# Kernel optimization log

Measured on AMD Instinct MI355X. Metric: run time of the kernel, lower is better.

Reference implementation:

```python
import jax, jax.numpy as jnp
import numpy as np

NV, NH = 6000, 6000
DV, DH = 1024, 1024
HID, HEADS = 128, 3
EV, EH, EC = 200000, 200000, 32768


def _gat(x, ei, W, a_src, a_dst, bias, edge_attr=None, lin_e=None, a_e=None):
    """PyG GATConv (heads=H, concat=False, add_self_loops=True, LeakyReLU 0.2).
    Returns (node_out [N,C], alpha [E+N, H])."""
    N = x.shape[0]
    H, C = a_src.shape
    xw = (x @ W).reshape(N, H, C)                      # [N,H,C]
    asrc = jnp.einsum('nhc,hc->nh', xw, a_src)         # [N,H]
    adst = jnp.einsum('nhc,hc->nh', xw, a_dst)
    loop = jnp.arange(N, dtype=ei.dtype)               # self-loops appended
    src = jnp.concatenate([ei[0], loop])
    dst = jnp.concatenate([ei[1], loop])
    alpha = asrc[src] + adst[dst]                      # [E+N,H]
    if edge_attr is not None:
        # edge_dim=1 path: lin_edge(weight)[E,H,C] dotted with att_edge; self-loop attr = mean (PyG fill_value='mean')
        ea = jnp.concatenate([edge_attr, jnp.full((N,), jnp.mean(edge_attr), edge_attr.dtype)])
        ef = (ea[:, None] * lin_e[None, :]).reshape(-1, H, C)
        alpha = alpha + jnp.einsum('ehc,hc->eh', ef, a_e)
    alpha = jax.nn.leaky_relu(alpha, 0.2)
    # segment softmax over incoming edges of each destination node
    amax = jax.ops.segment_max(alpha, dst, num_segments=N)
    ex = jnp.exp(alpha - amax[dst])
    den = jax.ops.segment_sum(ex, dst, num_segments=N)
    alpha = ex / (den[dst] + 1e-16)
    out = jax.ops.segment_sum(xw[src] * alpha[..., None], dst, num_segments=N)
    return out.mean(axis=1) + bias, alpha              # concat=False -> head mean


def _bn(x, g, b):  # BatchNorm1d, training mode (batch stats, biased var)
    m = x.mean(0)
    v = x.var(0)
    return (x - m) / jnp.sqrt(v + 1e-5) * g + b


def reference(virus_data, host_data, coexistence_data, virus_edge_weight, host_edge_weight,
              vW, v_asrc, v_adst, v_bias, v_line, v_atte,
              hW, h_asrc, h_adst, h_bias, h_line, h_atte,
              vhW, vh_asrc, vh_adst, vh_bias,
              hvW, hv_asrc, hv_adst, hv_bias,
              linv_W, linv_b, linh_W, linh_b, bn_g, bn_b,
              virus_edge_index, host_edge_index, coexistence_edge_index, coexistence_edge_index_t):
    feat_v, alpha_v = _gat(virus_data, virus_edge_index, vW, v_asrc, v_adst, v_bias,
                           virus_edge_weight, v_line, v_atte)
    feat_h, alpha_h = _gat(host_data, host_edge_index, hW, h_asrc, h_adst, h_bias,
                           host_edge_weight, h_line, h_atte)
    feat_vh, alpha_vh = _gat(coexistence_data, coexistence_edge_index_t, vhW, vh_asrc, vh_adst, vh_bias)
    feat_hv, alpha_hv = _gat(coexistence_data.T, coexistence_edge_index, hvW, hv_asrc, hv_adst, hv_bias)

    vh = jax.nn.leaky_relu(_bn(virus_data @ linv_W + linv_b, bn_g, bn_b), 0.01)
    hh = jax.nn.leaky_relu(_bn(host_data @ linh_W + linh_b, bn_g, bn_b), 0.01)

    output_host = vh @ hh.T                  # [Nv,Nh]
    output_virus = (hh @ vh.T).T             # [Nv,Nh]
    return (output_host, output_virus, output_host + output_virus,
            alpha_v, alpha_h, alpha_vh, alpha_hv,
            feat_v, feat_h, feat_vh, feat_hv)


def setup_inputs() -> dict:
    key = jax.random.key(0)
    ks = iter(jax.random.split(key, 48))

    def nrm(shape, s=0.05):
        return (jax.random.normal(next(ks), shape, jnp.float32) * s).astype(jnp.float32)

    def gat_params(din, edge=True):
        p = [nrm((din, HEADS * HID)), nrm((HEADS, HID)), nrm((HEADS, HID)), jnp.zeros((HID,), jnp.float32)]
        if edge:
            p += [nrm((HEADS * HID,)), nrm((HEADS, HID))]
        return p

    inp = {
        'virus_data': jax.random.normal(next(ks), (NV, DV), jnp.float32),
        'host_data': jax.random.normal(next(ks), (NH, DH), jnp.float32),
        'coexistence_data': jax.random.normal(next(ks), (DV, DH), jnp.float32),
        'virus_edge_weight': jax.random.uniform(next(ks), (EV,), jnp.float32),
        'host_edge_weight': jax.random.uniform(next(ks), (EH,), jnp.float32),
    }
    for pref, din, edge in [('v', DV, True), ('h', DH, True)]:
        W, asrc, adst, b, le, ae = gat_params(din, True)
        inp.update({f'{pref}W': W, f'{pref}_asrc': asrc, f'{pref}_adst': adst,
                    f'{pref}_bias': b, f'{pref}_line': le, f'{pref}_atte': ae})
    for pref, din in [('vh', DH), ('hv', DV)]:
        W, asrc, adst, b = gat_params(din, False)
        inp.update({f'{pref}W': W, f'{pref}_asrc': asrc, f'{pref}_adst': adst, f'{pref}_bias': b})
    inp.update({
        'linv_W': nrm((DV, HID)), 'linv_b': jnp.zeros((HID,), jnp.float32),
        'linh_W': nrm((DH, HID)), 'linh_b': jnp.zeros((HID,), jnp.float32),
        'bn_g': jnp.ones((HID,), jnp.float32), 'bn_b': jnp.zeros((HID,), jnp.float32),
        'virus_edge_index': jax.random.randint(next(ks), (2, EV), 0, NV, jnp.int32),
        'host_edge_index': jax.random.randint(next(ks), (2, EH), 0, NH, jnp.int32),
        'coexistence_edge_index': jax.random.randint(next(ks), (2, EC), 0, DH, jnp.int32),
        'coexistence_edge_index_t': jax.random.randint(next(ks), (2, EC), 0, DV, jnp.int32),
    })
    return inp
```

## Files before the change

kernel.cpp:

```cpp
#include <hip/hip_runtime.h>

#define NV   6000
#define NH   6000
#define EV   200000
#define EH   200000
#define EC   32768
#define GCAP 256

typedef __attribute__((ext_vector_type(8))) short bf16x8;
typedef __attribute__((ext_vector_type(4))) float f32x4;

__device__ __forceinline__ unsigned short f2bf(float f){
  unsigned u = __float_as_uint(f);
  u += 0x7FFFu + ((u >> 16) & 1u);
  return (unsigned short)(u >> 16);
}
__device__ __forceinline__ float bf2f(unsigned short h){
  return __uint_as_float((unsigned)h << 16);
}

__global__ __launch_bounds__(256) void k0(
    const float* __restrict__ vW, const float* __restrict__ v_as, const float* __restrict__ v_ad,
    const float* __restrict__ hW, const float* __restrict__ h_as, const float* __restrict__ h_ad,
    const float* __restrict__ vhW, const float* __restrict__ vh_as, const float* __restrict__ vh_ad,
    const float* __restrict__ hvW, const float* __restrict__ hv_as, const float* __restrict__ hv_ad,
    const float* __restrict__ vew, const float* __restrict__ hew,
    const float* __restrict__ v_line, const float* __restrict__ v_atte,
    const float* __restrict__ h_line, const float* __restrict__ h_atte,
    const int* __restrict__ vdst, const int* __restrict__ hdst,
    const int* __restrict__ c1dst, const int* __restrict__ c2dst,
    float* WasV, float* WadV, float* WasH, float* WadH,
    float* WasC1, float* WadC1, float* WasC2, float* WadC2,
    float* sums, float* Kbuf,
    int* cntV, int* cntH, int* cntC1, int* cntC2)
{
  __shared__ float red4[4][2];
  int b = blockIdx.x, t = threadIdx.x;
  int lane = t & 63, w = t >> 6;

  if (b < 2048){
    int m = b >> 9;
    int krow = (b & 511) * 2 + (t >> 7);
    int c = t & 127;
    const float *W, *as_, *ad_; float *Was, *Wad;
    switch (m){
      case 0:  W=vW;  as_=v_as;  ad_=v_ad;  Was=WasV;  Wad=WadV;  break;
      case 1:  W=hW;  as_=h_as;  ad_=h_ad;  Was=WasH;  Wad=WadH;  break;
      case 2:  W=vhW; as_=vh_as; ad_=vh_ad; Was=WasC1; Wad=WadC1; break;
      default: W=hvW; as_=hv_as; ad_=hv_ad; Was=WasC2; Wad=WadC2; break;
    }
    const float* Wr = W + (size_t)krow * 384;
    for (int h = 0; h < 3; h++){
      float x = Wr[h*128 + c];
      float s = x * as_[h*128 + c], d = x * ad_[h*128 + c];
      for (int off = 32; off > 0; off >>= 1){ s += __shfl_down(s, off); d += __shfl_down(d, off); }
      if (lane == 0){ red4[w][0] = s; red4[w][1] = d; }
      __syncthreads();
      if (t == 0)  { Was[krow*3+h] = red4[0][0] + red4[1][0]; Wad[krow*3+h] = red4[0][1] + red4[1][1]; }
      if (t == 128){ Was[krow*3+h] = red4[2][0] + red4[3][0]; Wad[krow*3+h] = red4[2][1] + red4[3][1]; }
      __syncthreads();
    }
    return;
  }
  b -= 2048;
  if (b < 1819){
    int idx = b * 256 + t;
    if (idx >= EV + EH + 2*EC) return;
    const int* dp; int* cnt; int e;
    if      (idx < EV)       { dp=vdst;  cnt=cntV;  e=idx; }
    else if (idx < EV+EH)    { dp=hdst;  cnt=cntH;  e=idx-EV; }
    else if (idx < EV+EH+EC) { dp=c1dst; cnt=cntC1; e=idx-EV-EH; }
    else                     { dp=c2dst; cnt=cntC2; e=idx-EV-EH-EC; }
    atomicAdd(&cnt[dp[e]], 1);
    return;
  }
  b -= 1819;
  if (b < 256){
    int which = b >> 7, base = b & 127;
    const float* x = which ? hew : vew;
    float s = 0.f;
    for (int i = base*256 + t; i < EV; i += 128*256) s += x[i];
    for (int off = 32; off > 0; off >>= 1) s += __shfl_down(s, off);
    if (lane == 0) red4[w][0] = s;
    __syncthreads();
    if (t == 0) atomicAdd(&sums[which], red4[0][0]+red4[1][0]+red4[2][0]+red4[3][0]);
    return;
  }
  for (int h = 0; h < 3; h++){
    float s = (t < 128) ? v_line[h*128+t] * v_atte[h*128+t] : 0.f;
    for (int off = 32; off > 0; off >>= 1) s += __shfl_down(s, off);
    if (lane == 0) red4[w][0] = s;
    __syncthreads();
    if (t == 0) Kbuf[h] = red4[0][0]+red4[1][0]+red4[2][0]+red4[3][0];
    __syncthreads();
    s = (t < 128) ? h_line[h*128+t] * h_atte[h*128+t] : 0.f;
    for (int off = 32; off > 0; off >>= 1) s += __shfl_down(s, off);
    if (lane == 0) red4[w][0] = s;
    __syncthreads();
    if (t == 0) Kbuf[3+h] = red4[0][0]+red4[1][0]+red4[2][0]+red4[3][0];
    __syncthreads();
  }
}

__global__ __launch_bounds__(256) void k_prep(
    const float* __restrict__ virus, const float* __restrict__ hostd, const float* __restrict__ coex,
    const float* __restrict__ vW, const float* __restrict__ linvW,
    const float* __restrict__ hW, const float* __restrict__ linhW,
    const float* __restrict__ vhW, const float* __restrict__ hvW,
    const float* __restrict__ WasV, const float* __restrict__ WadV,
    const float* __restrict__ WasH, const float* __restrict__ WadH,
    const float* __restrict__ WasC1, const float* __restrict__ WadC1,
    const float* __restrict__ WasC2, const float* __restrict__ WadC2,
    int* cntV, int* startsV, int* cntH, int* startsH,
    int* cntC1, int* startsC1, int* cntC2, int* startsC2,
    unsigned short* Avb, unsigned short* Ahb, unsigned short* Acb,
    unsigned short* Actb, unsigned short* BtV, unsigned short* BtH,
    unsigned short* BtVH, unsigned short* BtHV,
    float* asV, float* adV, float* asH, float* adH,
    float* asC1, float* adC1, float* asC2, float* adC2)
{
  __shared__ float scratch[64*65];
  int b = blockIdx.x, t = threadIdx.x;
  int lane = t & 63, w = t >> 6;

  if (b < 13024){
    const float* x; unsigned short* dstp; const float* Was; const float* Wad;
    float* ao; float* doo; int row;
    if (b < 6000)       { row=b;       x=virus; dstp=Avb; Was=WasV;  Wad=WadV;  ao=asV;  doo=adV; }
    else if (b < 12000) { row=b-6000;  x=hostd; dstp=Ahb; Was=WasH;  Wad=WadH;  ao=asH;  doo=adH; }
    else                { row=b-12000; x=coex;  dstp=Acb; Was=WasC1; Wad=WadC1; ao=asC1; doo=adC1; }
    float4 v = reinterpret_cast<const float4*>(x + (size_t)row * 1024)[t];
    ushort4 o; o.x = f2bf(v.x); o.y = f2bf(v.y); o.z = f2bf(v.z); o.w = f2bf(v.w);
    reinterpret_cast<ushort4*>(dstp + (size_t)row * 1024)[t] = o;
    const float4* Wp = reinterpret_cast<const float4*>(Was + t*12);
    float4 wa = Wp[0], wb = Wp[1], wcc = Wp[2];
    const float4* Dp = reinterpret_cast<const float4*>(Wad + t*12);
    float4 da = Dp[0], db = Dp[1], dcc = Dp[2];
    float r[6];
    r[0] = v.x*wa.x + v.y*wa.w + v.z*wb.z + v.w*wcc.y;
    r[1] = v.x*wa.y + v.y*wb.x + v.z*wb.w + v.w*wcc.z;
    r[2] = v.x*wa.z + v.y*wb.y + v.z*wcc.x + v.w*wcc.w;
    r[3] = v.x*da.x + v.y*da.w + v.z*db.z + v.w*dcc.y;
    r[4] = v.x*da.y + v.y*db.x + v.z*db.w + v.w*dcc.z;
    r[5] = v.x*da.z + v.y*db.y + v.z*dcc.x + v.w*dcc.w;
    for (int off = 32; off > 0; off >>= 1)
#pragma unroll
      for (int i = 0; i < 6; i++) r[i] += __shfl_down(r[i], off);
    float (*sh6)[6] = (float(*)[6])scratch;
    if (lane == 0)
#pragma unroll
      for (int i = 0; i < 6; i++) sh6[w][i] = r[i];
    __syncthreads();
    if (t < 6){
      float s = sh6[0][t] + sh6[1][t] + sh6[2][t] + sh6[3][t];
      if (t < 3) ao[row*3 + t] = s; else doo[row*3 + (t-3)] = s;
    }
    return;
  }
  b -= 13024;
  if (b < 704){
    float (*tp_lds)[65] = (float(*)[65])scratch;
    const float* src; unsigned short* dst; int Nc, roff, ntn, rel;
    if      (b < 256){ src=coex;  dst=Actb; Nc=1024; roff=0;   ntn=16; rel=b; }
    else if (b < 352){ src=vW;    dst=BtV;  Nc=384;  roff=0;   ntn=6;  rel=b-256; }
    else if (b < 384){ src=linvW; dst=BtV;  Nc=128;  roff=384; ntn=2;  rel=b-352; }
    else if (b < 480){ src=hW;    dst=BtH;  Nc=384;  roff=0;   ntn=6;  rel=b-384; }
    else if (b < 512){ src=linhW; dst=BtH;  Nc=128;  roff=384; ntn=2;  rel=b-480; }
    else if (b < 608){ src=vhW;   dst=BtVH; Nc=384;  roff=0;   ntn=6;  rel=b-512; }
    else             { src=hvW;   dst=BtHV; Nc=384;  roff=0;   ntn=6;  rel=b-608; }
    int tn = rel % ntn, tk = rel / ntn;
    int k0_ = tk * 64, n0 = tn * 64;
    int tx = t & 63, ty = t >> 6;
#pragma unroll
    for (int r = 0; r < 16; r++)
      tp_lds[ty + r*4][tx] = src[(size_t)(k0_ + ty + r*4) * Nc + n0 + tx];
    __syncthreads();
#pragma unroll
    for (int r = 0; r < 16; r++)
      dst[(size_t)(n0 + ty + r*4 + roff) * 1024 + k0_ + tx] = f2bf(tp_lds[tx][ty + r*4]);
    return;
  }
  b -= 704;
  if (b < 32){
    float (*st)[32][6] = (float(*)[32][6])scratch;
    int c = t & 31, ks = t >> 5;
    int nn = b * 32 + c;
    float a[6] = {0,0,0,0,0,0};
    for (int k = ks*128; k < ks*128 + 128; k++){
      float xv = coex[(size_t)k*1024 + nn];
      a[0] += xv*WasC2[k*3+0]; a[1] += xv*WasC2[k*3+1]; a[2] += xv*WasC2[k*3+2];
      a[3] += xv*WadC2[k*3+0]; a[4] += xv*WadC2[k*3+1]; a[5] += xv*WadC2[k*3+2];
    }
#pragma unroll
    for (int j = 0; j < 6; j++) st[ks][c][j] = a[j];
    __syncthreads();
    if (t < 32){
      float r[6] = {0,0,0,0,0,0};
#pragma unroll
      for (int k = 0; k < 8; k++)
#pragma unroll
        for (int j = 0; j < 6; j++) r[j] += st[k][t][j];
      int n2 = b * 32 + t;
      asC2[n2*3] = r[0]; asC2[n2*3+1] = r[1]; asC2[n2*3+2] = r[2];
      adC2[n2*3] = r[3]; adC2[n2*3+1] = r[4]; adC2[n2*3+2] = r[5];
    }
    return;
  }
  b -= 32;
  int* ssc = (int*)scratch;
  int* cnt; int* st_; int N;
  switch (b){
    case 0:  cnt=cntV;  st_=startsV;  N=NV;   break;
    case 1:  cnt=cntH;  st_=startsH;  N=NH;   break;
    case 2:  cnt=cntC1; st_=startsC1; N=1024; break;
    default: cnt=cntC2; st_=startsC2; N=1024; break;
  }
  int chunk = (N + 255) >> 8;
  int lo = t * chunk, hi = lo + chunk;
  if (hi > N) hi = N;
  if (lo > N) lo = N;
  int s = 0;
  for (int i = lo; i < hi; i++) s += cnt[i];
  ssc[t] = s;
  __syncthreads();
  for (int off = 1; off < 256; off <<= 1){
    int v = (t >= off) ? ssc[t - off] : 0;
    __syncthreads();
    ssc[t] += v;
    __syncthreads();
  }
  int run = ssc[t] - s;
  for (int i = lo; i < hi; i++){ st_[i] = run; run += cnt[i]; }
  if (t == 255) st_[N] = ssc[255];
}

template<int MODE>
__device__ __forceinline__ void gemm_body(
    const unsigned short* __restrict__ A, const unsigned short* __restrict__ B,
    int M, int N, unsigned short* __restrict__ xwb, float* __restrict__ lin,
    int bx, int by)
{
  const int tid  = threadIdx.x;
  const int lane = tid & 63, w = tid >> 6;
  const int wr = w >> 1, wc = w & 1;
  const int R  = by * 128 + wr * 64;
  const int Cb = bx * 64 + wc * 32;
  const int r0 = lane & 15, kg = lane >> 4;

  const unsigned short* pa[4]; const unsigned short* pb[2];
  bool va[4], vb[2];
#pragma unroll
  for (int i = 0; i < 4; i++){
    int row = R + i * 16 + r0;
    va[i] = row < M;
    pa[i] = A + (size_t)(va[i] ? row : 0) * 1024 + kg * 8;
  }
#pragma unroll
  for (int j = 0; j < 2; j++){
    int col = Cb + j * 16 + r0;
    vb[j] = col < N;
    pb[j] = B + (size_t)(vb[j] ? col : 0) * 1024 + kg * 8;
  }
  const bf16x8 Z8 = {0,0,0,0,0,0,0,0};
  f32x4 acc[4][2];
#pragma unroll
  for (int i = 0; i < 4; i++)
#pragma unroll
    for (int j = 0; j < 2; j++) acc[i][j] = (f32x4){0.f,0.f,0.f,0.f};

  for (int kk = 0; kk < 1024; kk += 32){
    bf16x8 av[4], bv[2];
#pragma unroll
    for (int i = 0; i < 4; i++){
      bf16x8 ta = *reinterpret_cast<const bf16x8*>(pa[i] + kk);
      av[i] = va[i] ? ta : Z8;
    }
#pragma unroll
    for (int j = 0; j < 2; j++){
      bf16x8 tb = *reinterpret_cast<const bf16x8*>(pb[j] + kk);
      bv[j] = vb[j] ? tb : Z8;
    }
#pragma unroll
    for (int i = 0; i < 4; i++)
#pragma unroll
      for (int j = 0; j < 2; j++)
        acc[i][j] = __builtin_amdgcn_mfma_f32_16x16x32_bf16(av[i], bv[j], acc[i][j], 0, 0, 0);
  }

  const int cn = lane & 15, rq = (lane >> 4) * 4;
#pragma unroll
  for (int i = 0; i < 4; i++){
    int row0 = R + i * 16 + rq;
#pragma unroll
    for (int j = 0; j < 2; j++){
      int col = Cb + j * 16 + cn;
      if (col < N){
#pragma unroll
        for (int r = 0; r < 4; r++){
          int row = row0 + r;
          if (row < M){
            float v = acc[i][j][r];
            if (MODE == 0){
              if (col < 384) xwb[(size_t)row * 384 + col] = f2bf(v);
              else           lin[(size_t)row * 128 + col - 384] = v;
            } else {
              xwb[(size_t)row * 384 + col] = f2bf(v);
            }
          }
        }
      }
    }
  }
}

__global__ __launch_bounds__(256) void k_sg(
    const unsigned short* Avb, const unsigned short* BtV, unsigned short* xwbV, float* linV,
    const unsigned short* Ahb, const unsigned short* BtH, unsigned short* xwbH, float* linH,
    const unsigned short* Acb,  const unsigned short* BtVH, unsigned short* xwbC1,
    const unsigned short* Actb, const unsigned short* BtHV, unsigned short* xwbC2,
    const int* vdst, const int* hdst, const int* c1dst, const int* c2dst,
    const int* stV, const int* stH, const int* st1, const int* st2,
    int* cuV, int* cuH, int* cu1, int* cu2,
    int* soV, int* soH, int* so1, int* so2)
{
  int b = blockIdx.x;
  if (b < 848){
    if (b < 376)       gemm_body<0>(Avb,  BtV,  NV,   512, xwbV,  linV, b & 7, b >> 3);
    else if (b < 752){ int g = b - 376; gemm_body<0>(Ahb,  BtH,  NH,   512, xwbH,  linH, g & 7, g >> 3); }
    else if (b < 800){ int g = b - 752; gemm_body<1>(Acb,  BtVH, 1024, 384, xwbC1, nullptr, g % 6, g / 6); }
    else             { int g = b - 800; gemm_body<1>(Actb, BtHV, 1024, 384, xwbC2, nullptr, g % 6, g / 6); }
    return;
  }
  int idx = (b - 848) * 256 + threadIdx.x;
  if (idx >= EV + EH + 2*EC) return;
  const int* dp; const int* st; int* cur; int* so; int e;
  if      (idx < EV)       { dp=vdst;  st=stV; cur=cuV; so=soV; e=idx; }
  else if (idx < EV+EH)    { dp=hdst;  st=stH; cur=cuH; so=soH; e=idx-EV; }
  else if (idx < EV+EH+EC) { dp=c1dst; st=st1; cur=cu1; so=so1; e=idx-EV-EH; }
  else                     { dp=c2dst; st=st2; cur=cu2; so=so2; e=idx-EV-EH-EC; }
  int d = dp[e];
  so[st[d] + atomicAdd(&cur[d], 1)] = e;
}

struct GatDesc {
  const unsigned short* xwb; const int* src; const int* sorted; const int* starts;
  const float* as_; const float* ad_; const float* Kc; const float* ew; const float* sumw;
  const float* bias; float* alpha; float* feat;
  int E; float invE;
};

__global__ __launch_bounds__(256) void k_gatbn(
    GatDesc dV, GatDesc dH, GatDesc d1, GatDesc d2,
    const float* __restrict__ linV, const float* __restrict__ linH, float* __restrict__ bnacc)
{
  int b = blockIdx.x, t = threadIdx.x;
  if (b >= 14048){
    int bb = b - 14048;
    int which = bb >= 188;
    int r0 = (which ? bb - 188 : bb) * 32 + (t >> 7) * 16;
    int c = t & 127;
    const float* lin = which ? linH : linV;
    float s = 0.f, q = 0.f;
#pragma unroll
    for (int r = 0; r < 16; r++){
      int row = r0 + r;
      if (row < NV){
        float v = lin[(size_t)row * 128 + c];
        s += v; q += v * v;
      }
    }
    atomicAdd(&bnacc[which*256 + c],       s);
    atomicAdd(&bnacc[which*256 + 128 + c], q);
    return;
  }
  GatDesc d; int n;
  if (b < 6000)       { d = dV; n = b; }
  else if (b < 12000) { d = dH; n = b - 6000; }
  else if (b < 13024) { d = d1; n = b - 12000; }
  else                { d = d2; n = b - 13024; }

  const int lane = t & 63, w = t >> 6;
  const int c = t & 127, half = t >> 7;
  __shared__ float shx[GCAP][3];
  __shared__ int   shs[GCAP];
  __shared__ float redm[4][3], reds[4][3], shD[128][3];

  const int s0  = d.starts[n];
  const int deg = d.starts[n+1] - s0;
  const bool hasW = (d.ew != nullptr);
  float K0=0.f, K1=0.f, K2=0.f, wself=0.f;
  if (hasW){ K0=d.Kc[0]; K1=d.Kc[1]; K2=d.Kc[2]; wself = d.sumw[0] * d.invE; }
  const float ad0 = d.ad_[n*3], ad1 = d.ad_[n*3+1], ad2 = d.ad_[n*3+2];
  float sr0 = d.as_[n*3+0] + ad0 + wself*K0;  sr0 = sr0 >= 0.f ? sr0 : 0.2f*sr0;
  float sr1 = d.as_[n*3+1] + ad1 + wself*K1;  sr1 = sr1 >= 0.f ? sr1 : 0.2f*sr1;
  float sr2 = d.as_[n*3+2] + ad2 + wself*K2;  sr2 = sr2 >= 0.f ? sr2 : 0.2f*sr2;

  float mx0 = sr0, mx1 = sr1, mx2 = sr2;
  for (int i = t; i < deg; i += 256){
    int e = d.sorted[s0 + i];
    int s = d.src[e];
    float wv = hasW ? d.ew[e] : 0.f;
    float r0 = d.as_[s*3+0] + ad0 + wv*K0;  r0 = r0 >= 0.f ? r0 : 0.2f*r0;
    float r1 = d.as_[s*3+1] + ad1 + wv*K1;  r1 = r1 >= 0.f ? r1 : 0.2f*r1;
    float r2 = d.as_[s*3+2] + ad2 + wv*K2;  r2 = r2 >= 0.f ? r2 : 0.2f*r2;
    if (i < GCAP){ shs[i] = s; shx[i][0]=r0; shx[i][1]=r1; shx[i][2]=r2; }
    mx0 = fmaxf(mx0, r0); mx1 = fmaxf(mx1, r1); mx2 = fmaxf(mx2, r2);
  }
  for (int off = 32; off > 0; off >>= 1){
    mx0 = fmaxf(mx0, __shfl_down(mx0, off));
    mx1 = fmaxf(mx1, __shfl_down(mx1, off));
    mx2 = fmaxf(mx2, __shfl_down(mx2, off));
  }
  if (lane == 0){ redm[w][0]=mx0; redm[w][1]=mx1; redm[w][2]=mx2; }
  __syncthreads();
  const float M0 = fmaxf(fmaxf(redm[0][0],redm[1][0]), fmaxf(redm[2][0],redm[3][0]));
  const float M1 = fmaxf(fmaxf(redm[0][1],redm[1][1]), fmaxf(redm[2][1],redm[3][1]));
  const float M2 = fmaxf(fmaxf(redm[0][2],redm[1][2]), fmaxf(redm[2][2],redm[3][2]));

  float t0 = 0.f, t1 = 0.f, t2 = 0.f;
  for (int i = t; i < deg; i += 256){
    float r0, r1, r2;
    if (i < GCAP){ r0 = shx[i][0]; r1 = shx[i][1]; r2 = shx[i][2]; }
    else {
      int e = d.sorted[s0 + i]; int s = d.src[e];
      float wv = hasW ? d.ew[e] : 0.f;
      r0 = d.as_[s*3+0]+ad0+wv*K0; r0 = r0>=0.f?r0:0.2f*r0;
      r1 = d.as_[s*3+1]+ad1+wv*K1; r1 = r1>=0.f?r1:0.2f*r1;
      r2 = d.as_[s*3+2]+ad2+wv*K2; r2 = r2>=0.f?r2:0.2f*r2;
    }
    float e0 = expf(r0 - M0), e1 = expf(r1 - M1), e2 = expf(r2 - M2);
    if (i < GCAP){ shx[i][0]=e0; shx[i][1]=e1; shx[i][2]=e2; }
    t0 += e0; t1 += e1; t2 += e2;
  }
  for (int off = 32; off > 0; off >>= 1){
    t0 += __shfl_down(t0, off); t1 += __shfl_down(t1, off); t2 += __shfl_down(t2, off);
  }
  if (lane == 0){ reds[w][0]=t0; reds[w][1]=t1; reds[w][2]=t2; }
  __syncthreads();
  const float se0 = expf(sr0 - M0), se1 = expf(sr1 - M1), se2 = expf(sr2 - M2);
  const float i0 = 1.f / (reds[0][0]+reds[1][0]+reds[2][0]+reds[3][0] + se0 + 1e-16f);
  const float i1 = 1.f / (reds[0][1]+reds[1][1]+reds[2][1]+reds[3][1] + se1 + 1e-16f);
  const float i2 = 1.f / (reds[0][2]+reds[1][2]+reds[2][2]+reds[3][2] + se2 + 1e-16f);

  for (int i = t; i < deg; i += 256){
    int e = d.sorted[s0 + i];
    float e0, e1, e2;
    if (i < GCAP){ e0 = shx[i][0]; e1 = shx[i][1]; e2 = shx[i][2]; }
    else {
      int s = d.src[e];
      float wv = hasW ? d.ew[e] : 0.f;
      float r0 = d.as_[s*3+0]+ad0+wv*K0; r0=r0>=0.f?r0:0.2f*r0;
      float r1 = d.as_[s*3+1]+ad1+wv*K1; r1=r1>=0.f?r1:0.2f*r1;
      float r2 = d.as_[s*3+2]+ad2+wv*K2; r2=r2>=0.f?r2:0.2f*r2;
      e0 = expf(r0-M0); e1 = expf(r1-M1); e2 = expf(r2-M2);
    }
    float* ap = d.alpha + (size_t)e * 3;
    ap[0] = e0 * i0; ap[1] = e1 * i1; ap[2] = e2 * i2;
  }
  if (t == 0){
    float* ap = d.alpha + (size_t)(d.E + n) * 3;
    ap[0] = se0 * i0; ap[1] = se1 * i1; ap[2] = se2 * i2;
  }

  float f0, f1, f2;
  if (half == 0){
    const unsigned short* xn = d.xwb + (size_t)n * 384;
    f0 = bf2f(xn[c]) * se0; f1 = bf2f(xn[128+c]) * se1; f2 = bf2f(xn[256+c]) * se2;
  } else { f0 = f1 = f2 = 0.f; }
  for (int i = half; i < deg; i += 2){
    int s; float e0, e1, e2;
    if (i < GCAP){ s = shs[i]; e0 = shx[i][0]; e1 = shx[i][1]; e2 = shx[i][2]; }
    else {
      int e = d.sorted[s0 + i]; s = d.src[e];
      float wv = hasW ? d.ew[e] : 0.f;
      float r0 = d.as_[s*3+0]+ad0+wv*K0; r0=r0>=0.f?r0:0.2f*r0;
      float r1 = d.as_[s*3+1]+ad1+wv*K1; r1=r1>=0.f?r1:0.2f*r1;
      float r2 = d.as_[s*3+2]+ad2+wv*K2; r2=r2>=0.f?r2:0.2f*r2;
      e0 = expf(r0-M0); e1 = expf(r1-M1); e2 = expf(r2-M2);
    }
    const unsigned short* xs = d.xwb + (size_t)s * 384;
    f0 += bf2f(xs[c]) * e0; f1 += bf2f(xs[128+c]) * e1; f2 += bf2f(xs[256+c]) * e2;
  }
  if (half == 1){ shD[c][0] = f0; shD[c][1] = f1; shD[c][2] = f2; }
  __syncthreads();
  if (half == 0){
    f0 += shD[c][0]; f1 += shD[c][1]; f2 += shD[c][2];
    d.feat[(size_t)n*128 + c] = (f0*i0 + f1*i1 + f2*i2) * (1.f/3.f) + d.bias[c];
  }
}

__global__ __launch_bounds__(256) void k_fin(
    const float* __restrict__ linV, const float* __restrict__ linH,
    const float* __restrict__ bnacc, const float* __restrict__ g, const float* __restrict__ bb,
    float* __restrict__ o0, float* __restrict__ o1, float* __restrict__ o2)
{
  __shared__ float sA[128], hA[128], sB[128], hB[128];
  const int t = threadIdx.x;
  if (t < 128){
    float mu  = bnacc[t] * (1.f/NV);
    float var = bnacc[128+t] * (1.f/NV) - mu*mu;
    float rs  = rsqrtf(var + 1e-5f);
    sA[t] = rs * g[t]; hA[t] = bb[t] - mu * rs * g[t];
  } else {
    int j = t - 128;
    float mu  = bnacc[256+j] * (1.f/NV);
    float var = bnacc[384+j] * (1.f/NV) - mu*mu;
    float rs  = rsqrtf(var + 1e-5f);
    sB[j] = rs * g[j]; hB[j] = bb[j] - mu * rs * g[j];
  }
  __syncthreads();

  const int lane = t & 63, w = t >> 6;
  const int wr = w >> 1, wc = w & 1;
  const int R  = blockIdx.y * 128 + wr * 64;
  const int Cb = blockIdx.x * 128 + wc * 64;
  const int r0 = lane & 15, kg = lane >> 4;

  const float* pa[4]; const float* pb[4];
  bool va[4], vb[4];
#pragma unroll
  for (int i = 0; i < 4; i++){
    int row = R + i * 16 + r0;
    va[i] = row < NV;
    pa[i] = linV + (size_t)(va[i] ? row : 0) * 128 + kg * 8;
    int col = Cb + i * 16 + r0;
    vb[i] = col < NH;
    pb[i] = linH + (size_t)(vb[i] ? col : 0) * 128 + kg * 8;
  }
  const bf16x8 Z8 = {0,0,0,0,0,0,0,0};
  f32x4 acc[4][4];
#pragma unroll
  for (int i = 0; i < 4; i++)
#pragma unroll
    for (int j = 0; j < 4; j++) acc[i][j] = (f32x4){0.f,0.f,0.f,0.f};

  for (int kk = 0; kk < 128; kk += 32){
    const int kb = kk + kg * 8;
    bf16x8 av[4], bv[4];
#pragma unroll
    for (int i = 0; i < 4; i++){
      bf16x8 fa, fb;
#pragma unroll
      for (int e = 0; e < 8; e++){
        float v1 = fmaf(pa[i][kk + e], sA[kb + e], hA[kb + e]);
        v1 = v1 >= 0.f ? v1 : 0.01f * v1;
        fa[e] = (short)f2bf(v1);
        float v2 = fmaf(pb[i][kk + e], sB[kb + e], hB[kb + e]);
        v2 = v2 >= 0.f ? v2 : 0.01f * v2;
        fb[e] = (short)f2bf(v2);
      }
      av[i] = va[i] ? fa : Z8;
      bv[i] = vb[i] ? fb : Z8;
    }
#pragma unroll
    for (int i = 0; i < 4; i++)
#pragma unroll
      for (int j = 0; j < 4; j++)
        acc[i][j] = __builtin_amdgcn_mfma_f32_16x16x32_bf16(av[i], bv[j], acc[i][j], 0, 0, 0);
  }

  const int cn = lane & 15, rq = (lane >> 4) * 4;
#pragma unroll
  for (int i = 0; i < 4; i++){
    int row0 = R + i * 16 + rq;
#pragma unroll
    for (int j = 0; j < 4; j++){
      int col = Cb + j * 16 + cn;
      if (col < NH){
#pragma unroll
        for (int r = 0; r < 4; r++){
          int row = row0 + r;
          if (row < NV){
            size_t idx = (size_t)row * NH + col;
            float v = acc[i][j][r];
            o0[idx] = v; o1[idx] = v; o2[idx] = v + v;
          }
        }
      }
    }
  }
}

extern "C" void kernel_launch(void* const* d_in, const int* in_sizes, int n_in,
                              void* d_out, int out_size, void* d_ws, size_t ws_size,
                              hipStream_t stream)
{
  (void)in_sizes; (void)n_in; (void)out_size; (void)ws_size;
  const float* virus  = (const float*)d_in[0];
  const float* hostd  = (const float*)d_in[1];
  const float* coex   = (const float*)d_in[2];
  const float* vew    = (const float*)d_in[3];
  const float* hew    = (const float*)d_in[4];
  const float* vW     = (const float*)d_in[5];
  const float* v_as   = (const float*)d_in[6];
  const float* v_ad   = (const float*)d_in[7];
  const float* v_bias = (const float*)d_in[8];
  const float* v_line = (const float*)d_in[9];
  const float* v_atte = (const float*)d_in[10];
  const float* hW     = (const float*)d_in[11];
  const float* h_as   = (const float*)d_in[12];
  const float* h_ad   = (const float*)d_in[13];
  const float* h_bias = (const float*)d_in[14];
  const float* h_line = (const float*)d_in[15];
  const float* h_atte = (const float*)d_in[16];
  const float* vhW    = (const float*)d_in[17];
  const float* vh_as  = (const float*)d_in[18];
  const float* vh_ad  = (const float*)d_in[19];
  const float* vh_bias= (const float*)d_in[20];
  const float* hvW    = (const float*)d_in[21];
  const float* hv_as  = (const float*)d_in[22];
  const float* hv_ad  = (const float*)d_in[23];
  const float* hv_bias= (const float*)d_in[24];
  const float* linvW  = (const float*)d_in[25];
  const float* linhW  = (const float*)d_in[27];
  const float* bng    = (const float*)d_in[29];
  const float* bnb    = (const float*)d_in[30];
  const int* vei  = (const int*)d_in[31];
  const int* hei  = (const int*)d_in[32];
  const int* cei  = (const int*)d_in[33];
  const int* ceit = (const int*)d_in[34];

  float* out = (float*)d_out;
  float* o0 = out;
  float* o1 = out + 36000000ll;
  float* o2 = out + 72000000ll;
  float* alpha_v  = out + 108000000ll;
  float* alpha_h  = alpha_v  + 618000;
  float* alpha_vh = alpha_h  + 618000;
  float* alpha_hv = alpha_vh + 101376;
  float* feat_v   = alpha_hv + 101376;
  float* feat_h   = feat_v   + 768000;
  float* feat_vh  = feat_h   + 768000;
  float* feat_hv  = feat_vh  + 131072;

  char* wp = (char*)d_ws;
  auto alloc = [&](size_t b) -> void* { void* p = wp; wp += (b + 255) & ~(size_t)255; return p; };
  unsigned short* Avb  = (unsigned short*)alloc((size_t)NV*1024*2);
  unsigned short* Ahb  = (unsigned short*)alloc((size_t)NH*1024*2);
  unsigned short* Acb  = (unsigned short*)alloc((size_t)1024*1024*2);
  unsigned short* Actb = (unsigned short*)alloc((size_t)1024*1024*2);
  unsigned short* BtV  = (unsigned short*)alloc((size_t)512*1024*2);
  unsigned short* BtH  = (unsigned short*)alloc((size_t)512*1024*2);
  unsigned short* BtVH = (unsigned short*)alloc((size_t)384*1024*2);
  unsigned short* BtHV = (unsigned short*)alloc((size_t)384*1024*2);
  unsigned short* xwbV = (unsigned short*)alloc((size_t)NV*384*2);
  unsigned short* xwbH = (unsigned short*)alloc((size_t)NH*384*2);
  unsigned short* xwbC1= (unsigned short*)alloc((size_t)1024*384*2);
  unsigned short* xwbC2= (unsigned short*)alloc((size_t)1024*384*2);
  float* linV = (float*)alloc((size_t)NV*128*4);
  float* linH = (float*)alloc((size_t)NH*128*4);
  float* asV  = (float*)alloc(NV*3*4);   float* adV  = (float*)alloc(NV*3*4);
  float* asH  = (float*)alloc(NH*3*4);   float* adH  = (float*)alloc(NH*3*4);
  float* asC1 = (float*)alloc(1024*3*4); float* adC1 = (float*)alloc(1024*3*4);
  float* asC2 = (float*)alloc(1024*3*4); float* adC2 = (float*)alloc(1024*3*4);
  float* WasV = (float*)alloc(1024*3*4); float* WadV = (float*)alloc(1024*3*4);
  float* WasH = (float*)alloc(1024*3*4); float* WadH = (float*)alloc(1024*3*4);
  float* WasC1= (float*)alloc(1024*3*4); float* WadC1= (float*)alloc(1024*3*4);
  float* WasC2= (float*)alloc(1024*3*4); float* WadC2= (float*)alloc(1024*3*4);
  int* startsV  = (int*)alloc((NV+1)*4);  int* sortedV  = (int*)alloc((size_t)EV*4);
  int* startsH  = (int*)alloc((NH+1)*4);  int* sortedH  = (int*)alloc((size_t)EH*4);
  int* startsC1 = (int*)alloc(1025*4);    int* sortedC1 = (int*)alloc((size_t)EC*4);
  int* startsC2 = (int*)alloc(1025*4);    int* sortedC2 = (int*)alloc((size_t)EC*4);
  float* Kbuf  = (float*)alloc(256);
  char* z0 = wp;
  int* cntV  = (int*)alloc(NV*4);   int* curV  = (int*)alloc(NV*4);
  int* cntH  = (int*)alloc(NH*4);   int* curH  = (int*)alloc(NH*4);
  int* cntC1 = (int*)alloc(1024*4); int* curC1 = (int*)alloc(1024*4);
  int* cntC2 = (int*)alloc(1024*4); int* curC2 = (int*)alloc(1024*4);
  float* sums  = (float*)alloc(256);
  float* bnacc = (float*)alloc(512*4);
  hipMemsetAsync(z0, 0, (size_t)(wp - z0), stream);

  const int* vsrc = vei,  *vdst = vei  + EV;
  const int* hsrc = hei,  *hdst = hei  + EH;
  const int* c1src= ceit, *c1dst= ceit + EC;
  const int* c2src= cei,  *c2dst= cei  + EC;

  k0<<<4124, 256, 0, stream>>>(vW, v_as, v_ad, hW, h_as, h_ad,
      vhW, vh_as, vh_ad, hvW, hv_as, hv_ad,
      vew, hew, v_line, v_atte, h_line, h_atte,
      vdst, hdst, c1dst, c2dst,
      WasV, WadV, WasH, WadH, WasC1, WadC1, WasC2, WadC2,
      sums, Kbuf, cntV, cntH, cntC1, cntC2);
  k_prep<<<13764, 256, 0, stream>>>(virus, hostd, coex,
      vW, linvW, hW, linhW, vhW, hvW,
      WasV, WadV, WasH, WadH, WasC1, WadC1, WasC2, WadC2,
      cntV, startsV, cntH, startsH, cntC1, startsC1, cntC2, startsC2,
      Avb, Ahb, Acb, Actb, BtV, BtH, BtVH, BtHV,
      asV, adV, asH, adH, asC1, adC1, asC2, adC2);
  k_sg<<<2667, 256, 0, stream>>>(Avb, BtV, xwbV, linV, Ahb, BtH, xwbH, linH,
      Acb, BtVH, xwbC1, Actb, BtHV, xwbC2,
      vdst, hdst, c1dst, c2dst,
      startsV, startsH, startsC1, startsC2,
      curV, curH, curC1, curC2,
      sortedV, sortedH, sortedC1, sortedC2);
  {
    GatDesc dv = { xwbV,  vsrc,  sortedV,  startsV,  asV,  adV,  Kbuf,   vew, &sums[0], v_bias,
                   alpha_v,  feat_v,  EV, 1.f/EV };
    GatDesc dh = { xwbH,  hsrc,  sortedH,  startsH,  asH,  adH,  Kbuf+3, hew, &sums[1], h_bias,
                   alpha_h,  feat_h,  EH, 1.f/EH };
    GatDesc dc1= { xwbC1, c1src, sortedC1, startsC1, asC1, adC1, nullptr, nullptr, nullptr, vh_bias,
                   alpha_vh, feat_vh, EC, 0.f };
    GatDesc dc2= { xwbC2, c2src, sortedC2, startsC2, asC2, adC2, nullptr, nullptr, nullptr, hv_bias,
                   alpha_hv, feat_hv, EC, 0.f };
    k_gatbn<<<14424, 256, 0, stream>>>(dv, dh, dc1, dc2, linV, linH, bnacc);
  }
  k_fin<<<dim3(47,47), 256, 0, stream>>>(linV, linH, bnacc, bng, bnb, o0, o1, o2);
}
```

Before: 837.3 us.

## Stage GEMM tiles through double-buffered LDS with register prefetch

The fused GEMM body used to have every wave load its A and B fragments straight from global memory, so the two column waves and two row waves read the same data twice. Each block now loads its 128x32 A tile and 64x32 B tile into shared memory once per k-step. The tiles are double-buffered, and the next tile is prefetched into registers while the MFMAs run. This cuts redundant global traffic and hides load latency, at the cost of 24KB of LDS per block and a barrier per k-step. The shared arrays are also allocated in the edge-sorting blocks, which may reduce their occupancy.

```diff
diff --git a/kernel.cpp b/kernel.cpp
--- a/kernel.cpp
+++ b/kernel.cpp
@@ -238,62 +238,78 @@
 __device__ __forceinline__ void gemm_body(
     const unsigned short* __restrict__ A, const unsigned short* __restrict__ B,
     int M, int N, unsigned short* __restrict__ xwb, float* __restrict__ lin,
-    int bx, int by)
+    int bx, int by, unsigned short* As, unsigned short* Bs)
 {
   const int tid  = threadIdx.x;
-  const int lane = tid & 63, w = tid >> 6;
-  const int wr = w >> 1, wc = w & 1;
-  const int R  = by * 128 + wr * 64;
-  const int Cb = bx * 64 + wc * 32;
+  const int lane = tid & 63, wv = tid >> 6;
+  const int wr = wv >> 1, wc = wv & 1;
+  const int R  = by * 128;
+  const int Cb = bx * 64;
   const int r0 = lane & 15, kg = lane >> 4;
 
-  const unsigned short* pa[4]; const unsigned short* pb[2];
-  bool va[4], vb[2];
+  const int ar0 = tid >> 2;
+  const int ac  = (tid & 3) * 8;
+  int gra0 = R + ar0;        if (gra0 >= M) gra0 = M - 1;
+  int gra1 = R + ar0 + 64;   if (gra1 >= M) gra1 = M - 1;
+  const unsigned short* pa0 = A + (size_t)gra0 * 1024 + ac;
+  const unsigned short* pa1 = A + (size_t)gra1 * 1024 + ac;
+  const unsigned short* pb  = B + (size_t)(Cb + ar0) * 1024 + ac;
+
+  f32x4 acc[4][2];
+#pragma unroll
+  for (int i = 0; i < 4; i++)
+#pragma unroll
+    for (int j = 0; j < 2; j++) acc[i][j] = (f32x4){0.f,0.f,0.f,0.f};
+
+  bf16x8 nA0 = *reinterpret_cast<const bf16x8*>(pa0);
+  bf16x8 nA1 = *reinterpret_cast<const bf16x8*>(pa1);
+  bf16x8 nB  = *reinterpret_cast<const bf16x8*>(pb);
+  *reinterpret_cast<bf16x8*>(&As[ar0*32 + ac])      = nA0;
+  *reinterpret_cast<bf16x8*>(&As[(ar0+64)*32 + ac]) = nA1;
+  *reinterpret_cast<bf16x8*>(&Bs[ar0*32 + ac])      = nB;
+  __syncthreads();
+
+  int cur = 0;
+  for (int kt = 0; kt < 32; ++kt){
+    const int kn = (kt + 1) * 32;
+    if (kt < 31){
+      nA0 = *reinterpret_cast<const bf16x8*>(pa0 + kn);
+      nA1 = *reinterpret_cast<const bf16x8*>(pa1 + kn);
+      nB  = *reinterpret_cast<const bf16x8*>(pb  + kn);
+    }
+    unsigned short* Ab = As + cur * 4096;
+    unsigned short* Bb = Bs + cur * 2048;
+    bf16x8 af[4], bfr[2];
+#pragma unroll
+    for (int i = 0; i < 4; i++)
+      af[i] = *reinterpret_cast<const bf16x8*>(&Ab[(wr*64 + i*16 + r0)*32 + kg*8]);
+#pragma unroll
+    for (int j = 0; j < 2; j++)
+      bfr[j] = *reinterpret_cast<const bf16x8*>(&Bb[(wc*32 + j*16 + r0)*32 + kg*8]);
+#pragma unroll
+    for (int i = 0; i < 4; i++)
+#pragma unroll
+      for (int j = 0; j < 2; j++)
+        acc[i][j] = __builtin_amdgcn_mfma_f32_16x16x32_bf16(af[i], bfr[j], acc[i][j], 0, 0, 0);
+    if (kt < 31){
+      int nxt = cur ^ 1;
+      unsigned short* An = As + nxt * 4096;
+      unsigned short* Bn = Bs + nxt * 2048;
+      *reinterpret_cast<bf16x8*>(&An[ar0*32 + ac])      = nA0;
+      *reinterpret_cast<bf16x8*>(&An[(ar0+64)*32 + ac]) = nA1;
+      *reinterpret_cast<bf16x8*>(&Bn[ar0*32 + ac])      = nB;
+      __syncthreads();
+      cur = nxt;
+    }
+  }
+
+  const int cn = lane & 15, rq = (lane >> 4) * 4;
 #pragma unroll
   for (int i = 0; i < 4; i++){
-    int row = R + i * 16 + r0;
-    va[i] = row < M;
-    pa[i] = A + (size_t)(va[i] ? row : 0) * 1024 + kg * 8;
-  }
-#pragma unroll
-  for (int j = 0; j < 2; j++){
-    int col = Cb + j * 16 + r0;
-    vb[j] = col < N;
-    pb[j] = B + (size_t)(vb[j] ? col : 0) * 1024 + kg * 8;
-  }
-  const bf16x8 Z8 = {0,0,0,0,0,0,0,0};
-  f32x4 acc[4][2];
-#pragma unroll
-  for (int i = 0; i < 4; i++)
-#pragma unroll
-    for (int j = 0; j < 2; j++) acc[i][j] = (f32x4){0.f,0.f,0.f,0.f};
-
-  for (int kk = 0; kk < 1024; kk += 32){
-    bf16x8 av[4], bv[2];
-#pragma unroll
-    for (int i = 0; i < 4; i++){
-      bf16x8 ta = *reinterpret_cast<const bf16x8*>(pa[i] + kk);
-      av[i] = va[i] ? ta : Z8;
-    }
+    int row0 = R + wr*64 + i * 16 + rq;
 #pragma unroll
     for (int j = 0; j < 2; j++){
-      bf16x8 tb = *reinterpret_cast<const bf16x8*>(pb[j] + kk);
-      bv[j] = vb[j] ? tb : Z8;
-    }
-#pragma unroll
-    for (int i = 0; i < 4; i++)
-#pragma unroll
-      for (int j = 0; j < 2; j++)
-        acc[i][j] = __builtin_amdgcn_mfma_f32_16x16x32_bf16(av[i], bv[j], acc[i][j], 0, 0, 0);
-  }
-
-  const int cn = lane & 15, rq = (lane >> 4) * 4;
-#pragma unroll
-  for (int i = 0; i < 4; i++){
-    int row0 = R + i * 16 + rq;
-#pragma unroll
-    for (int j = 0; j < 2; j++){
-      int col = Cb + j * 16 + cn;
+      int col = Cb + wc*32 + j * 16 + cn;
       if (col < N){
 #pragma unroll
         for (int r = 0; r < 4; r++){
@@ -323,12 +339,14 @@
     int* cuV, int* cuH, int* cu1, int* cu2,
     int* soV, int* soH, int* so1, int* so2)
 {
+  __shared__ unsigned short As[2*4096];
+  __shared__ unsigned short Bs[2*2048];
   int b = blockIdx.x;
   if (b < 848){
-    if (b < 376)       gemm_body<0>(Avb,  BtV,  NV,   512, xwbV,  linV, b & 7, b >> 3);
-    else if (b < 752){ int g = b - 376; gemm_body<0>(Ahb,  BtH,  NH,   512, xwbH,  linH, g & 7, g >> 3); }
-    else if (b < 800){ int g = b - 752; gemm_body<1>(Acb,  BtVH, 1024, 384, xwbC1, nullptr, g % 6, g / 6); }
-    else             { int g = b - 800; gemm_body<1>(Actb, BtHV, 1024, 384, xwbC2, nullptr, g % 6, g / 6); }
+    if (b < 376)       gemm_body<0>(Avb,  BtV,  NV,   512, xwbV,  linV, b & 7, b >> 3, As, Bs);
+    else if (b < 752){ int g = b - 376; gemm_body<0>(Ahb,  BtH,  NH,   512, xwbH,  linH, g & 7, g >> 3, As, Bs); }
+    else if (b < 800){ int g = b - 752; gemm_body<1>(Acb,  BtVH, 1024, 384, xwbC1, nullptr, g % 6, g / 6, As, Bs); }
+    else             { int g = b - 800; gemm_body<1>(Actb, BtHV, 1024, 384, xwbC2, nullptr, g % 6, g / 6, As, Bs); }
     return;
   }
   int idx = (b - 848) * 256 + threadIdx.x;
```

New measurement: 810.2 us. 3.2% less time.
